# Optimization experiments

Hardware: AMD Instinct MI355X
Metric: run time of the kernel (lower is better)

Reference implementation:

```python
import jax, jax.numpy as jnp
import numpy as np

N_NODES = 50000
N_EDGES = 800000
ATOM_F = 64
NBR_F = 64
EPS = 1e-5


def batch_norm(x, gamma, beta):
    # BatchNorm1d in training mode: batch stats, biased variance
    mu = x.mean(axis=0)
    var = x.var(axis=0)
    return gamma * (x - mu) * jax.lax.rsqrt(var + EPS) + beta


def setup_inputs() -> dict:
    key = jax.random.key(0)
    ks = jax.random.split(key, 8)
    d_in = 2 * ATOM_F + NBR_F  # 192
    d_out = 2 * ATOM_F         # 128
    return {
        "atom_in_fea": jax.random.normal(ks[0], (N_NODES, ATOM_F), dtype=jnp.float32),
        "nbr_fea": jax.random.normal(ks[1], (N_EDGES, NBR_F), dtype=jnp.float32),
        "edge_src": jax.random.randint(ks[2], (N_EDGES,), 0, N_NODES),
        "edge_dst": jax.random.randint(ks[3], (N_EDGES,), 0, N_NODES),
        "W_full": jax.random.normal(ks[4], (d_in, d_out), dtype=jnp.float32) / np.sqrt(d_in),
        "b_full": jnp.zeros((d_out,), dtype=jnp.float32),
        "bn1_g": jnp.ones((d_out,), dtype=jnp.float32),
        "bn1_b": jnp.zeros((d_out,), dtype=jnp.float32),
        "bn2_g": jnp.ones((ATOM_F,), dtype=jnp.float32),
        "bn2_b": jnp.zeros((ATOM_F,), dtype=jnp.float32),
    }


def reference(atom_in_fea, nbr_fea, edge_src, edge_dst,
              W_full, b_full, bn1_g, bn1_b, bn2_g, bn2_b):
    # gather endpoint features per edge: [E, 2*A + Nf]
    atom_src = atom_in_fea[edge_src]
    atom_dst = atom_in_fea[edge_dst]
    total = jnp.concatenate([atom_src, atom_dst, nbr_fea], axis=1)
    total = batch_norm(total @ W_full + b_full, bn1_g, bn1_b)  # [E, 2*A]
    filter_fea, core_fea = jnp.split(total, 2, axis=1)
    nbr_msg = jax.nn.sigmoid(filter_fea) * jax.nn.softplus(core_fea)  # [E, A]
    # scatter-add messages back to destination nodes
    atom_update = jax.ops.segment_sum(nbr_msg, edge_dst, num_segments=atom_in_fea.shape[0])
    return jax.nn.softplus(atom_in_fea + batch_norm(atom_update, bn2_g, bn2_b))
```

## Files before the change

kernel.cpp:

```cpp
#include <hip/hip_runtime.h>
#include <hip/hip_fp16.h>
#include <math.h>

#define N_NODES 50000
#define N_EDGES 800000
#define ATOMF 64
#define DIN 192
#define DOUT 128
#define EPB 64
#define NTILES (N_EDGES / EPB)
#define LDW 200
#define ZLD 136

typedef __attribute__((ext_vector_type(8))) short bf16x8;
typedef __attribute__((ext_vector_type(8))) short s16x8;
typedef __attribute__((ext_vector_type(4))) float f32x4;

__device__ __forceinline__ short f2bf(float f) {
  unsigned u = __float_as_uint(f);
  u += 0x7fffu + ((u >> 16) & 1u);
  return (short)(u >> 16);
}
__device__ __forceinline__ unsigned short f2h(float f) {
  __half h = __float2half_rn(f);
  return *(unsigned short*)&h;
}
__device__ __forceinline__ float h2f(unsigned short u) {
  __half h = *(__half*)&u;
  return __half2float(h);
}
__device__ __forceinline__ float softplus_f(float x) {
  return fmaxf(x, 0.f) + log1pf(__expf(-fabsf(x)));
}
__device__ __forceinline__ float sigmoid_f(float x) {
  return 1.f / (1.f + __expf(-x));
}
__device__ __forceinline__ float fast_sigmoid(float x) {
  return __builtin_amdgcn_rcpf(1.f + __expf(-x));
}
__device__ __forceinline__ float fast_softplus(float x) {
  return fmaxf(x, 0.f) + __logf(1.f + __expf(-fabsf(x)));
}

__launch_bounds__(256)
__global__ void precvt_k(const float* __restrict__ atom,
                         const float* __restrict__ nbr,
                         const int* __restrict__ edst,
                         unsigned short* __restrict__ atom_bf,
                         unsigned short* __restrict__ nbr_bf,
                         int* __restrict__ deg) {
  const int NA = N_NODES * ATOMF / 8;
  const int NB = N_EDGES * ATOMF / 8;
  int gid = blockIdx.x * blockDim.x + threadIdx.x;
  int stride = gridDim.x * blockDim.x;
  if (deg) {
    for (int i = gid; i < N_EDGES; i += stride) atomicAdd(&deg[edst[i]], 1);
  }
  for (int i = gid; i < NA + NB; i += stride) {
    const float* s;
    unsigned short* d;
    if (i < NA) { s = atom + (size_t)i * 8; d = atom_bf + (size_t)i * 8; }
    else        { s = nbr + (size_t)(i - NA) * 8; d = nbr_bf + (size_t)(i - NA) * 8; }
    float4 a = ((const float4*)s)[0];
    float4 b = ((const float4*)s)[1];
    s16x8 t;
    t[0] = f2bf(a.x); t[1] = f2bf(a.y); t[2] = f2bf(a.z); t[3] = f2bf(a.w);
    t[4] = f2bf(b.x); t[5] = f2bf(b.y); t[6] = f2bf(b.z); t[7] = f2bf(b.w);
    *(s16x8*)d = t;
  }
}

__launch_bounds__(1024)
__global__ void scan_k(const int* __restrict__ deg,
                       int* __restrict__ rowptr,
                       int* __restrict__ cursor) {
  __shared__ int wsum[16];
  const int tid = threadIdx.x;
  const int lane = tid & 63, wv = tid >> 6;
  const int N4 = N_NODES / 4;
  int base = 0;
  for (int c0 = 0; c0 < N4; c0 += 1024) {
    int i4 = c0 + tid;
    int4 v = make_int4(0, 0, 0, 0);
    if (i4 < N4) v = ((const int4*)deg)[i4];
    int t = v.x + v.y + v.z + v.w;
    int s = t;
    #pragma unroll
    for (int d = 1; d < 64; d <<= 1) {
      int u = __shfl_up(s, d, 64);
      if (lane >= d) s += u;
    }
    if (lane == 63) wsum[wv] = s;
    __syncthreads();
    if (wv == 0 && lane < 16) {
      int ws = wsum[lane];
      #pragma unroll
      for (int d = 1; d < 16; d <<= 1) {
        int u = __shfl_up(ws, d, 64);
        if (lane >= d) ws += u;
      }
      wsum[lane] = ws;
    }
    __syncthreads();
    int wbase = wv ? wsum[wv - 1] : 0;
    int excl = base + wbase + s - t;
    if (i4 < N4) {
      int4 r;
      r.x = excl;
      r.y = excl + v.x;
      r.z = r.y + v.y;
      r.w = r.z + v.z;
      ((int4*)rowptr)[i4] = r;
      ((int4*)cursor)[i4] = r;
    }
    int tot = wsum[15];
    __syncthreads();
    base += tot;
  }
  if (tid == 0) rowptr[N_NODES] = base;
}

__launch_bounds__(256)
__global__ void fill_k(const int* __restrict__ edst,
                       int* __restrict__ cursor,
                       int* __restrict__ iperm) {
  int gid = blockIdx.x * 256 + threadIdx.x;
  if (gid < N_EDGES) {
    int pos = atomicAdd(&cursor[edst[gid]], 1);
    iperm[gid] = pos;
  }
}

__launch_bounds__(256, 4)
__global__ void edge_gemm(const unsigned short* __restrict__ atom_bf,
                          const unsigned short* __restrict__ nbr_bf,
                          const int* __restrict__ esrc,
                          const int* __restrict__ edst,
                          const int* __restrict__ iperm,
                          const float* __restrict__ W,
                          float* __restrict__ stats,
                          unsigned short* __restrict__ zc) {
  __shared__ unsigned short Zl[EPB * ZLD];

  const int tid = threadIdx.x;
  const int lane = tid & 63;
  const int wv = tid >> 6;
  const int l15 = lane & 15;
  const int lg = lane >> 4;
  const int colF = wv * 16 + l15;
  const int colC = colF + 64;

  bf16x8 wf[2][6];
  #pragma unroll
  for (int cg = 0; cg < 2; ++cg) {
    #pragma unroll
    for (int kk = 0; kk < 6; ++kk) {
      bf16x8 t;
      #pragma unroll
      for (int jj = 0; jj < 8; ++jj)
        t[jj] = f2bf(W[(size_t)(kk * 32 + lg * 8 + jj) * 128 + cg * 64 + colF]);
      wf[cg][kk] = t;
    }
  }

  const int orow = tid >> 2;
  const int oq = tid & 3;

  float fs[2] = {0.f, 0.f}, fq[2] = {0.f, 0.f};

  for (int tile = blockIdx.x; tile < NTILES; tile += gridDim.x) {
    const int e0 = tile * EPB;

    f32x4 acc[2][4] = {};
    #pragma unroll
    for (int rg = 0; rg < 4; ++rg) {
      int e = e0 + rg * 16 + l15;
      const unsigned short* srcb = atom_bf + (size_t)esrc[e] * ATOMF + lg * 8;
      const unsigned short* dstb = atom_bf + (size_t)edst[e] * ATOMF + lg * 8;
      const unsigned short* nbrb = nbr_bf + (size_t)e * ATOMF + lg * 8;
      bf16x8 a0 = *(const bf16x8*)srcb;
      bf16x8 a1 = *(const bf16x8*)(srcb + 32);
      bf16x8 a2 = *(const bf16x8*)dstb;
      bf16x8 a3 = *(const bf16x8*)(dstb + 32);
      bf16x8 a4 = *(const bf16x8*)nbrb;
      bf16x8 a5 = *(const bf16x8*)(nbrb + 32);
      acc[0][rg] = __builtin_amdgcn_mfma_f32_16x16x32_bf16(a0, wf[0][0], acc[0][rg], 0, 0, 0);
      acc[1][rg] = __builtin_amdgcn_mfma_f32_16x16x32_bf16(a0, wf[1][0], acc[1][rg], 0, 0, 0);
      acc[0][rg] = __builtin_amdgcn_mfma_f32_16x16x32_bf16(a1, wf[0][1], acc[0][rg], 0, 0, 0);
      acc[1][rg] = __builtin_amdgcn_mfma_f32_16x16x32_bf16(a1, wf[1][1], acc[1][rg], 0, 0, 0);
      acc[0][rg] = __builtin_amdgcn_mfma_f32_16x16x32_bf16(a2, wf[0][2], acc[0][rg], 0, 0, 0);
      acc[1][rg] = __builtin_amdgcn_mfma_f32_16x16x32_bf16(a2, wf[1][2], acc[1][rg], 0, 0, 0);
      acc[0][rg] = __builtin_amdgcn_mfma_f32_16x16x32_bf16(a3, wf[0][3], acc[0][rg], 0, 0, 0);
      acc[1][rg] = __builtin_amdgcn_mfma_f32_16x16x32_bf16(a3, wf[1][3], acc[1][rg], 0, 0, 0);
      acc[0][rg] = __builtin_amdgcn_mfma_f32_16x16x32_bf16(a4, wf[0][4], acc[0][rg], 0, 0, 0);
      acc[1][rg] = __builtin_amdgcn_mfma_f32_16x16x32_bf16(a4, wf[1][4], acc[1][rg], 0, 0, 0);
      acc[0][rg] = __builtin_amdgcn_mfma_f32_16x16x32_bf16(a5, wf[0][5], acc[0][rg], 0, 0, 0);
      acc[1][rg] = __builtin_amdgcn_mfma_f32_16x16x32_bf16(a5, wf[1][5], acc[1][rg], 0, 0, 0);
    }

    #pragma unroll
    for (int cg = 0; cg < 2; ++cg) {
      #pragma unroll
      for (int rg = 0; rg < 4; ++rg) {
        float z0 = acc[cg][rg][0], z1 = acc[cg][rg][1];
        float z2 = acc[cg][rg][2], z3 = acc[cg][rg][3];
        fs[cg] += (z0 + z1) + (z2 + z3);
        fq[cg] += z0 * z0 + z1 * z1 + z2 * z2 + z3 * z3;
      }
    }

    __syncthreads();

    #pragma unroll
    for (int cg = 0; cg < 2; ++cg)
      #pragma unroll
      for (int rg = 0; rg < 4; ++rg)
        #pragma unroll
        for (int r = 0; r < 4; ++r)
          Zl[(rg * 16 + lg * 4 + r) * ZLD + cg * 64 + colF] = f2h(acc[cg][rg][r]);

    __syncthreads();

    {
      int pos = iperm[tile * 64 + orow];
      const s16x8* src = (const s16x8*)&Zl[orow * ZLD + oq * 32];
      s16x8 v0 = src[0], v1 = src[1], v2 = src[2], v3 = src[3];
      unsigned short* dst = zc + (size_t)pos * 128 + oq * 32;
      *(s16x8*)dst = v0;
      *(s16x8*)(dst + 8) = v1;
      *(s16x8*)(dst + 16) = v2;
      *(s16x8*)(dst + 24) = v3;
    }
  }

  #pragma unroll
  for (int cg = 0; cg < 2; ++cg) {
    fs[cg] += __shfl_xor(fs[cg], 16, 64); fs[cg] += __shfl_xor(fs[cg], 32, 64);
    fq[cg] += __shfl_xor(fq[cg], 16, 64); fq[cg] += __shfl_xor(fq[cg], 32, 64);
  }
  if (lane < 16) {
    atomicAdd(&stats[colF], fs[0]);
    atomicAdd(&stats[colC], fs[1]);
    atomicAdd(&stats[128 + colF], fq[0]);
    atomicAdd(&stats[128 + colC], fq[1]);
  }
}

__global__ void finalize1_k(const float* __restrict__ stats,
                            const float* __restrict__ g,
                            const float* __restrict__ be,
                            float* __restrict__ ab) {
  int n = threadIdx.x;
  float mu = stats[n] * (1.f / N_EDGES);
  float var = stats[128 + n] * (1.f / N_EDGES) - mu * mu;
  float a = g[n] * rsqrtf(var + 1e-5f);
  ab[n] = a;
  ab[128 + n] = be[n] - mu * a;
}

__launch_bounds__(256)
__global__ void gather_k(const unsigned short* __restrict__ zc,
                         const int* __restrict__ rowptr,
                         const float* __restrict__ ab,
                         float* __restrict__ out,
                         float* __restrict__ stats2) {
  const int nwaves = gridDim.x * 4;
  const int wgid = blockIdx.x * 4 + (threadIdx.x >> 6);
  const int c = threadIdx.x & 63;
  float af = ab[c], cf = ab[128 + c];
  float ag = ab[64 + c], cg2 = ab[192 + c];
  float s2 = 0.f, q2 = 0.f;
  for (int n = wgid; n < N_NODES; n += nwaves) {
    int s = rowptr[n], e = rowptr[n + 1];
    float acc = 0.f;
    int i = s;
    for (; i + 2 <= e; i += 2) {
      const unsigned short* r0 = zc + (size_t)i * 128;
      const unsigned short* r1 = r0 + 128;
      float f0 = af * h2f(r0[c]) + cf;
      float g0 = ag * h2f(r0[64 + c]) + cg2;
      float f1 = af * h2f(r1[c]) + cf;
      float g1 = ag * h2f(r1[64 + c]) + cg2;
      acc += fast_sigmoid(f0) * fast_softplus(g0);
      acc += fast_sigmoid(f1) * fast_softplus(g1);
    }
    if (i < e) {
      const unsigned short* r0 = zc + (size_t)i * 128;
      float f0 = af * h2f(r0[c]) + cf;
      float g0 = ag * h2f(r0[64 + c]) + cg2;
      acc += fast_sigmoid(f0) * fast_softplus(g0);
    }
    out[(size_t)n * 64 + c] = acc;
    s2 += acc;
    q2 += acc * acc;
  }
  __shared__ float red[4 * 128];
  int wv = threadIdx.x >> 6;
  red[wv * 128 + c] = s2;
  red[wv * 128 + 64 + c] = q2;
  __syncthreads();
  int tid = threadIdx.x;
  if (tid < 128) {
    float v = red[tid] + red[128 + tid] + red[256 + tid] + red[384 + tid];
    atomicAdd(&stats2[tid], v);
  }
}

__launch_bounds__(256)
__global__ void stats2_k(const float* __restrict__ upd, float* __restrict__ stats2) {
  int tid = threadIdx.x;
  int gid = blockIdx.x * 256 + tid;
  int stride = gridDim.x * 256;
  float4 s = make_float4(0.f, 0.f, 0.f, 0.f);
  float4 q = make_float4(0.f, 0.f, 0.f, 0.f);
  for (int i = gid; i < N_NODES * 16; i += stride) {
    float4 v = ((const float4*)upd)[i];
    s.x += v.x; s.y += v.y; s.z += v.z; s.w += v.w;
    q.x += v.x * v.x; q.y += v.y * v.y; q.z += v.z * v.z; q.w += v.w * v.w;
  }
  int lane = tid & 63;
  int wv = tid >> 6;
  s.x += __shfl_xor(s.x, 16, 64); s.x += __shfl_xor(s.x, 32, 64);
  s.y += __shfl_xor(s.y, 16, 64); s.y += __shfl_xor(s.y, 32, 64);
  s.z += __shfl_xor(s.z, 16, 64); s.z += __shfl_xor(s.z, 32, 64);
  s.w += __shfl_xor(s.w, 16, 64); s.w += __shfl_xor(s.w, 32, 64);
  q.x += __shfl_xor(q.x, 16, 64); q.x += __shfl_xor(q.x, 32, 64);
  q.y += __shfl_xor(q.y, 16, 64); q.y += __shfl_xor(q.y, 32, 64);
  q.z += __shfl_xor(q.z, 16, 64); q.z += __shfl_xor(q.z, 32, 64);
  q.w += __shfl_xor(q.w, 16, 64); q.w += __shfl_xor(q.w, 32, 64);
  __shared__ float red[4 * 128];
  if (lane < 16) {
    int f = lane * 4;
    red[wv * 128 + f + 0] = s.x; red[wv * 128 + f + 1] = s.y;
    red[wv * 128 + f + 2] = s.z; red[wv * 128 + f + 3] = s.w;
    red[wv * 128 + 64 + f + 0] = q.x; red[wv * 128 + 64 + f + 1] = q.y;
    red[wv * 128 + 64 + f + 2] = q.z; red[wv * 128 + 64 + f + 3] = q.w;
  }
  __syncthreads();
  if (tid < 128) {
    float v = red[tid] + red[128 + tid] + red[256 + tid] + red[384 + tid];
    atomicAdd(&stats2[tid], v);
  }
}

__launch_bounds__(256)
__global__ void out_k(const float* __restrict__ atom,
                      const float* __restrict__ stats2,
                      const float* __restrict__ g2,
                      const float* __restrict__ b2,
                      float* __restrict__ out) {
  int gid = blockIdx.x * 256 + threadIdx.x;
  int stride = gridDim.x * 256;
  for (int i = gid; i < N_NODES * 16; i += stride) {
    float4 u = ((const float4*)out)[i];
    float4 x = ((const float4*)atom)[i];
    int f = (i & 15) * 4;
    float a[4], bb[4];
    #pragma unroll
    for (int k = 0; k < 4; ++k) {
      float mu = stats2[f + k] * (1.f / N_NODES);
      float var = stats2[64 + f + k] * (1.f / N_NODES) - mu * mu;
      a[k] = g2[f + k] * rsqrtf(var + 1e-5f);
      bb[k] = b2[f + k] - mu * a[k];
    }
    float4 r;
    r.x = softplus_f(x.x + u.x * a[0] + bb[0]);
    r.y = softplus_f(x.y + u.y * a[1] + bb[1]);
    r.z = softplus_f(x.z + u.z * a[2] + bb[2]);
    r.w = softplus_f(x.w + u.w * a[3] + bb[3]);
    ((float4*)out)[i] = r;
  }
}

template<int PASS>
__launch_bounds__(256, 2)
__global__ void edge_pass(const float* __restrict__ atom,
                          const float* __restrict__ nbr,
                          const int* __restrict__ esrc,
                          const int* __restrict__ edst,
                          const float* __restrict__ W,
                          const float* __restrict__ bvec,
                          float* __restrict__ stats,
                          const float* __restrict__ ab,
                          float* __restrict__ upd) {
  __shared__ short Wl[DOUT * LDW];
  __shared__ short Tl[EPB * LDW];
  __shared__ int eix[2 * EPB];

  const int tid = threadIdx.x;
  const int lane = tid & 63;
  const int wv = tid >> 6;
  const int l15 = lane & 15;
  const int lg = lane >> 4;

  for (int i = tid; i < DIN * DOUT; i += 256) {
    int k = i >> 7, n = i & 127;
    Wl[n * LDW + k] = f2bf(W[i]);
  }
  float bcol[8], acol[8], ccol[8];
  #pragma unroll
  for (int j = 0; j < 8; ++j) {
    int n = j * 16 + l15;
    bcol[j] = bvec[n];
    if constexpr (PASS == 1) { acol[j] = ab[n]; ccol[j] = ab[DOUT + n]; }
    else { acol[j] = 0.f; ccol[j] = 0.f; }
  }
  float fsum[8], fsq[8];
  #pragma unroll
  for (int j = 0; j < 8; ++j) { fsum[j] = 0.f; fsq[j] = 0.f; }

  for (int tile = blockIdx.x; tile < NTILES; tile += gridDim.x) {
    const int e0 = tile * EPB;
    __syncthreads();
    if (tid < EPB) eix[tid] = esrc[e0 + tid];
    else if (tid < 2 * EPB) eix[tid] = edst[e0 + tid - EPB];
    __syncthreads();
    for (int i = tid; i < EPB * 96; i += 256) {
      int row = i / 96;
      int cl = (i - row * 96) * 2;
      const float* p;
      if (cl < 64)       p = atom + (size_t)eix[row] * 64 + cl;
      else if (cl < 128) p = atom + (size_t)eix[EPB + row] * 64 + (cl - 64);
      else               p = nbr + (size_t)(e0 + row) * 64 + (cl - 128);
      float2 v = *(const float2*)p;
      unsigned pk = (unsigned)(unsigned short)f2bf(v.x)
                  | ((unsigned)(unsigned short)f2bf(v.y) << 16);
      *(unsigned*)&Tl[row * LDW + cl] = pk;
    }
    __syncthreads();
    f32x4 acc[8] = {};
    const int abase = (wv * 16 + l15) * LDW + lg * 8;
    #pragma unroll
    for (int kk = 0; kk < 6; ++kk) {
      bf16x8 afr = *(const bf16x8*)&Tl[abase + kk * 32];
      #pragma unroll
      for (int j = 0; j < 8; ++j) {
        bf16x8 bfr = *(const bf16x8*)&Wl[(j * 16 + l15) * LDW + lg * 8 + kk * 32];
        acc[j] = __builtin_amdgcn_mfma_f32_16x16x32_bf16(afr, bfr, acc[j], 0, 0, 0);
      }
    }
    if constexpr (PASS == 0) {
      #pragma unroll
      for (int j = 0; j < 8; ++j)
        #pragma unroll
        for (int r = 0; r < 4; ++r) {
          float z = acc[j][r] + bcol[j];
          fsum[j] += z; fsq[j] += z * z;
        }
    } else {
      #pragma unroll
      for (int r = 0; r < 4; ++r) {
        int row = wv * 16 + lg * 4 + r;
        int d = eix[EPB + row];
        float* urow = upd + (size_t)d * 64;
        #pragma unroll
        for (int j = 0; j < 4; ++j) {
          float f = (acc[j][r] + bcol[j]) * acol[j] + ccol[j];
          float g = (acc[j + 4][r] + bcol[j + 4]) * acol[j + 4] + ccol[j + 4];
          atomicAdd(&urow[j * 16 + l15], sigmoid_f(f) * softplus_f(g));
        }
      }
    }
  }
  if constexpr (PASS == 0) {
    #pragma unroll
    for (int j = 0; j < 8; ++j) {
      fsum[j] += __shfl_xor(fsum[j], 16, 64);
      fsum[j] += __shfl_xor(fsum[j], 32, 64);
      fsq[j]  += __shfl_xor(fsq[j], 16, 64);
      fsq[j]  += __shfl_xor(fsq[j], 32, 64);
    }
    __syncthreads();
    float* redf = (float*)Tl;
    if (lane < 16) {
      #pragma unroll
      for (int j = 0; j < 8; ++j) {
        redf[wv * 256 + j * 16 + lane] = fsum[j];
        redf[wv * 256 + 128 + j * 16 + lane] = fsq[j];
      }
    }
    __syncthreads();
    float s = redf[tid] + redf[256 + tid] + redf[512 + tid] + redf[768 + tid];
    atomicAdd(&stats[tid], s);
  }
}

extern "C" void kernel_launch(void* const* d_in, const int* in_sizes, int n_in,
                              void* d_out, int out_size, void* d_ws, size_t ws_size,
                              hipStream_t stream) {
  const float* atom = (const float*)d_in[0];
  const float* nbr  = (const float*)d_in[1];
  const int*   esrc = (const int*)d_in[2];
  const int*   edst = (const int*)d_in[3];
  const float* W    = (const float*)d_in[4];
  const float* bvec = (const float*)d_in[5];
  const float* g1   = (const float*)d_in[6];
  const float* b1   = (const float*)d_in[7];
  const float* g2   = (const float*)d_in[8];
  const float* b2   = (const float*)d_in[9];
  float* out = (float*)d_out;
  char* ws = (char*)d_ws;

  float* stats1 = (float*)ws;
  float* ab1    = stats1 + 256;
  float* stats2 = stats1 + 512;

  const size_t OFF_ATOM = 4096;
  const size_t SZ_ATOM  = (size_t)N_NODES * ATOMF * 2;
  const size_t OFF_NBR  = OFF_ATOM + SZ_ATOM;
  const size_t SZ_NBR   = (size_t)N_EDGES * ATOMF * 2;
  const size_t OFF_ZT   = OFF_NBR + SZ_NBR;
  const size_t SZ_ZT    = (size_t)N_EDGES * DOUT * 2;
  const size_t OFF_PERM = OFF_ZT + SZ_ZT;
  const size_t SZ_PERM  = (size_t)N_EDGES * 4;
  const size_t OFF_DEG  = OFF_PERM + SZ_PERM;
  const size_t OFF_RP   = OFF_DEG + N_NODES * 4;
  const size_t OFF_CUR  = OFF_RP + (N_NODES + 1) * 4 + 12;
  const size_t NEED_NEW = OFF_CUR + N_NODES * 4;

  hipMemsetAsync(stats1, 0, 768 * sizeof(float), stream);

  if (ws_size >= NEED_NEW) {
    unsigned short* atom_bf = (unsigned short*)(ws + OFF_ATOM);
    unsigned short* nbr_bf  = (unsigned short*)(ws + OFF_NBR);
    unsigned short* zc      = (unsigned short*)(ws + OFF_ZT);
    int* iperm  = (int*)(ws + OFF_PERM);
    int* deg    = (int*)(ws + OFF_DEG);
    int* rowptr = (int*)(ws + OFF_RP);
    int* cursor = (int*)(ws + OFF_CUR);

    hipMemsetAsync(deg, 0, N_NODES * sizeof(int), stream);
    precvt_k<<<2048, 256, 0, stream>>>(atom, nbr, edst, atom_bf, nbr_bf, deg);
    scan_k<<<1, 1024, 0, stream>>>(deg, rowptr, cursor);
    fill_k<<<(N_EDGES + 255) / 256, 256, 0, stream>>>(edst, cursor, iperm);

    edge_gemm<<<1024, 256, 0, stream>>>(atom_bf, nbr_bf, esrc, edst, iperm,
                                        W, stats1, zc);
    finalize1_k<<<1, 128, 0, stream>>>(stats1, g1, b1, ab1);

    gather_k<<<1024, 256, 0, stream>>>(zc, rowptr, ab1, out, stats2);
  } else {
    hipMemsetAsync(out, 0, (size_t)N_NODES * 64 * sizeof(float), stream);
    edge_pass<0><<<512, 256, 0, stream>>>(atom, nbr, esrc, edst, W, bvec,
                                          stats1, nullptr, nullptr);
    finalize1_k<<<1, 128, 0, stream>>>(stats1, g1, b1, ab1);
    edge_pass<1><<<512, 256, 0, stream>>>(atom, nbr, esrc, edst, W, bvec,
                                          nullptr, ab1, out);
    stats2_k<<<512, 256, 0, stream>>>(out, stats2);
  }

  out_k<<<512, 256, 0, stream>>>(atom, stats2, g2, b2, out);
}
```

Baseline: 465.4 us.

## Use one wave per node with paired half loads in gather, move BN2 stats out

The gather kernel now assigns one wave per destination node through a large grid instead of grid-striding. Each lane loads 32-bit pairs of fp16 values and swaps halves with a cross-lane shuffle, so each lane computes two channels. The fused BatchNorm-2 statistics reduction and its atomics are removed from gather and done by the separate stats2_k kernel, which adds one extra read of the output. Half the lanes do redundant activation math, and one extra launch is added.

```diff
diff --git a/kernel.cpp b/kernel.cpp
--- a/kernel.cpp
+++ b/kernel.cpp
@@ -262,48 +262,53 @@
 __global__ void gather_k(const unsigned short* __restrict__ zc,
                          const int* __restrict__ rowptr,
                          const float* __restrict__ ab,
-                         float* __restrict__ out,
-                         float* __restrict__ stats2) {
-  const int nwaves = gridDim.x * 4;
-  const int wgid = blockIdx.x * 4 + (threadIdx.x >> 6);
-  const int c = threadIdx.x & 63;
-  float af = ab[c], cf = ab[128 + c];
-  float ag = ab[64 + c], cg2 = ab[192 + c];
-  float s2 = 0.f, q2 = 0.f;
-  for (int n = wgid; n < N_NODES; n += nwaves) {
-    int s = rowptr[n], e = rowptr[n + 1];
-    float acc = 0.f;
-    int i = s;
-    for (; i + 2 <= e; i += 2) {
-      const unsigned short* r0 = zc + (size_t)i * 128;
-      const unsigned short* r1 = r0 + 128;
-      float f0 = af * h2f(r0[c]) + cf;
-      float g0 = ag * h2f(r0[64 + c]) + cg2;
-      float f1 = af * h2f(r1[c]) + cf;
-      float g1 = ag * h2f(r1[64 + c]) + cg2;
-      acc += fast_sigmoid(f0) * fast_softplus(g0);
-      acc += fast_sigmoid(f1) * fast_softplus(g1);
-    }
-    if (i < e) {
-      const unsigned short* r0 = zc + (size_t)i * 128;
-      float f0 = af * h2f(r0[c]) + cf;
-      float g0 = ag * h2f(r0[64 + c]) + cg2;
-      acc += fast_sigmoid(f0) * fast_softplus(g0);
-    }
-    out[(size_t)n * 64 + c] = acc;
-    s2 += acc;
-    q2 += acc * acc;
-  }
-  __shared__ float red[4 * 128];
-  int wv = threadIdx.x >> 6;
-  red[wv * 128 + c] = s2;
-  red[wv * 128 + 64 + c] = q2;
-  __syncthreads();
-  int tid = threadIdx.x;
-  if (tid < 128) {
-    float v = red[tid] + red[128 + tid] + red[256 + tid] + red[384 + tid];
-    atomicAdd(&stats2[tid], v);
-  }
+                         float* __restrict__ out) {
+  int n = blockIdx.x * 4 + (threadIdx.x >> 6);
+  if (n >= N_NODES) return;
+  const int lane = threadIdx.x & 63;
+  const int lp = lane & 31;
+  const bool hi = lane >= 32;
+  const int c0 = 2 * lp, c1 = 2 * lp + 1;
+  float af0 = ab[c0], cf0 = ab[128 + c0];
+  float ag0 = ab[64 + c0], cg0 = ab[192 + c0];
+  float af1 = ab[c1], cf1 = ab[128 + c1];
+  float ag1 = ab[64 + c1], cg1 = ab[192 + c1];
+  int s = rowptr[n], e = rowptr[n + 1];
+  float a0 = 0.f, a1 = 0.f;
+  int i = s;
+  for (; i + 2 <= e; i += 2) {
+    unsigned v0 = *(const unsigned*)(zc + (size_t)i * 128 + lane * 2);
+    unsigned v1 = *(const unsigned*)(zc + (size_t)(i + 1) * 128 + lane * 2);
+    unsigned o0 = __shfl_xor((int)v0, 32, 64);
+    unsigned o1 = __shfl_xor((int)v1, 32, 64);
+    unsigned fv0 = hi ? o0 : v0, gv0 = hi ? v0 : o0;
+    unsigned fv1 = hi ? o1 : v1, gv1 = hi ? v1 : o1;
+    float f00 = af0 * h2f((unsigned short)(fv0 & 0xffff)) + cf0;
+    float f01 = af1 * h2f((unsigned short)(fv0 >> 16)) + cf1;
+    float g00 = ag0 * h2f((unsigned short)(gv0 & 0xffff)) + cg0;
+    float g01 = ag1 * h2f((unsigned short)(gv0 >> 16)) + cg1;
+    float f10 = af0 * h2f((unsigned short)(fv1 & 0xffff)) + cf0;
+    float f11 = af1 * h2f((unsigned short)(fv1 >> 16)) + cf1;
+    float g10 = ag0 * h2f((unsigned short)(gv1 & 0xffff)) + cg0;
+    float g11 = ag1 * h2f((unsigned short)(gv1 >> 16)) + cg1;
+    a0 += fast_sigmoid(f00) * fast_softplus(g00);
+    a1 += fast_sigmoid(f01) * fast_softplus(g01);
+    a0 += fast_sigmoid(f10) * fast_softplus(g10);
+    a1 += fast_sigmoid(f11) * fast_softplus(g11);
+  }
+  if (i < e) {
+    unsigned v0 = *(const unsigned*)(zc + (size_t)i * 128 + lane * 2);
+    unsigned o0 = __shfl_xor((int)v0, 32, 64);
+    unsigned fv0 = hi ? o0 : v0, gv0 = hi ? v0 : o0;
+    float f00 = af0 * h2f((unsigned short)(fv0 & 0xffff)) + cf0;
+    float f01 = af1 * h2f((unsigned short)(fv0 >> 16)) + cf1;
+    float g00 = ag0 * h2f((unsigned short)(gv0 & 0xffff)) + cg0;
+    float g01 = ag1 * h2f((unsigned short)(gv0 >> 16)) + cg1;
+    a0 += fast_sigmoid(f00) * fast_softplus(g00);
+    a1 += fast_sigmoid(f01) * fast_softplus(g01);
+  }
+  if (!hi)
+    *(float2*)(out + (size_t)n * 64 + c0) = make_float2(a0, a1);
 }
 
 __launch_bounds__(256)
@@ -538,7 +543,8 @@
                                         W, stats1, zc);
     finalize1_k<<<1, 128, 0, stream>>>(stats1, g1, b1, ab1);
 
-    gather_k<<<1024, 256, 0, stream>>>(zc, rowptr, ab1, out, stats2);
+    gather_k<<<(N_NODES + 3) / 4, 256, 0, stream>>>(zc, rowptr, ab1, out);
+    stats2_k<<<512, 256, 0, stream>>>(out, stats2);
   } else {
     hipMemsetAsync(out, 0, (size_t)N_NODES * 64 * sizeof(float), stream);
     edge_pass<0><<<512, 256, 0, stream>>>(atom, nbr, esrc, edst, W, bvec,
```

Measured after the change: 469.8 us. About the same (+1.0%).
